# Performance work log

Measured on AMD Instinct MI355X. Metric: run time of the kernel, lower is better.

## Reference

```python
import jax, jax.numpy as jnp
import numpy as np

B, L, E, Fm, Y, K = 16, 2500, 100, 50, 8921, 10
PAD = K // 2  # floor(kernel_size/2) = 5; even kernel -> output length L+1, as in torch


def setup_inputs() -> dict:
    key = jax.random.key(0)
    ks = jax.random.split(key, 6)
    x = jax.random.normal(ks[0], (B, L, E), dtype=jnp.float32)
    target = (jax.random.uniform(ks[1], (B, Y)) < 0.01).astype(jnp.float32)
    conv_w = jax.random.normal(ks[2], (Fm, E, K), dtype=jnp.float32) * 0.05  # (out, in, k)
    conv_b = jnp.zeros((Fm,), jnp.float32)
    U_w = jax.random.normal(ks[3], (Y, Fm), dtype=jnp.float32) * 0.05
    final_w = jax.random.normal(ks[4], (Y, Fm), dtype=jnp.float32) * 0.05
    final_b = jnp.zeros((Y,), jnp.float32)
    return dict(x=x, target=target, conv_w=conv_w, conv_b=conv_b,
                U_w=U_w, final_w=final_w, final_b=final_b)


def reference(x, target, conv_w, conv_b, U_w, final_w, final_b):
    # dropout is identity in eval mode
    xc = jnp.transpose(x, (0, 2, 1))  # (B, E, L)
    h = jax.lax.conv_general_dilated(
        xc, conv_w, window_strides=(1,), padding=[(PAD, PAD)],
        dimension_numbers=('NCH', 'OIH', 'NCH'))  # (B, Fm, L+1)
    h = jnp.tanh(jnp.transpose(h + conv_b[None, :, None], (0, 2, 1)))  # (B, Lp, Fm)
    # label-wise attention: U.weight @ h^T -> (B, Y, Lp)
    scores = jnp.einsum('yf,blf->byl', U_w, h)
    alpha = jax.nn.softmax(scores, axis=2)          # (B, Y, Lp) -- dominant memory traffic
    m = jnp.einsum('byl,blf->byf', alpha, h)        # (B, Y, Fm)
    logits = jnp.sum(final_w[None, :, :] * m, axis=2) + final_b  # (B, Y)
    proba = jax.nn.log_softmax(logits, axis=1)
    # binary_cross_entropy_with_logits, mean reduction (numerically stable form)
    loss = jnp.mean(jnp.maximum(logits, 0) - logits * target
                    + jnp.log1p(jnp.exp(-jnp.abs(logits))))
    return proba, loss, alpha
```

## Files before the change

kernel.cpp:

```cpp
#include <hip/hip_runtime.h>
#include <math.h>

#define Bn 16
#define Ln 2500
#define En 100
#define FM 50
#define Yn 8921
#define KS 10
#define LP 2501
#define NT 40
#define TILE_BYTES 19456
#define TILE_SHORTS 9728
#define HT_OFF 5120
#define CH_FULL 19
#define CH_A 10
#define NW 8
#define YB 128
#define NYB 70

typedef __attribute__((ext_vector_type(8))) short short8;
typedef __attribute__((ext_vector_type(4))) float f32x4;

union S8 { short8 v; long l2[2]; short s[8]; };

__device__ __forceinline__ short f2bf(float f){
  unsigned u = __float_as_uint(f);
  unsigned r = (u + 0x7fffu + ((u >> 16) & 1u)) >> 16;
  return (short)r;
}

__device__ __forceinline__ void g2l16(const void* g, void* l){
  __builtin_amdgcn_global_load_lds(
      (const __attribute__((address_space(1))) unsigned int*)g,
      (__attribute__((address_space(3))) unsigned int*)l, 16, 0, 0);
}

__device__ __forceinline__ void stage_chunks(const char* __restrict__ gbase,
                                             char* lbase, int wave, int lane,
                                             int nch, int nw){
  for (int chunk = wave; chunk < nch; chunk += nw)
    g2l16(gbase + chunk * 1024 + lane * 16, lbase + chunk * 1024 + lane * 16);
}

__global__ void k0_wt(const float* __restrict__ cw, float* __restrict__ WT){
  int i = blockIdx.x * 256 + threadIdx.x;
  if (i < 64000){
    int f = i & 63, ek = i >> 6;
    WT[i] = (f < FM) ? cw[f * 1000 + ek] : 0.f;
  }
}

__global__ __launch_bounds__(256) void k1_conv(
    const float* __restrict__ x, const float* __restrict__ WT,
    const float* __restrict__ conv_b, short* __restrict__ Hp)
{
  int id = blockIdx.x;
  int xcd = id & 7, rr = id >> 3;
  int b   = xcd + ((rr >= NT) ? 8 : 0);
  int t   = (rr >= NT) ? rr - NT : rr;
  int tid = threadIdx.x;
  __shared__ float x_s[100 * 76];
  __shared__ short h_t[64 * 69];

  int r0 = 64 * t - 5;
  for (int d = tid; d < 7300; d += 256){
    int row = d / 100, e = d - row * 100;
    int gr = r0 + row;
    float v = (gr >= 0 && gr < Ln) ? x[((size_t)b * Ln + gr) * 100 + e] : 0.f;
    x_s[e * 76 + row] = v;
  }
  __syncthreads();

  int f = tid & 63, lsub = tid >> 6;
  float acc[16];
#pragma unroll
  for (int j = 0; j < 16; j++) acc[j] = 0.f;

  for (int e = 0; e < 100; e++){
    float xv[25];
    const float* xr = x_s + e * 76 + lsub * 16;
#pragma unroll
    for (int i = 0; i < 6; i++){
      f32x4 q = *(const f32x4*)(xr + 4 * i);
      xv[4*i+0] = q[0]; xv[4*i+1] = q[1]; xv[4*i+2] = q[2]; xv[4*i+3] = q[3];
    }
    xv[24] = xr[24];
#pragma unroll
    for (int k = 0; k < KS; k++){
      float wv = WT[(e * 10 + k) * 64 + f];
#pragma unroll
      for (int j = 0; j < 16; j++) acc[j] += wv * xv[j + k];
    }
  }

  float bias = (f < FM) ? conv_b[f] : 0.f;
  size_t tbS = (size_t)(b * NT + t) * TILE_SHORTS;
#pragma unroll
  for (int j = 0; j < 16; j++){
    int l = lsub * 16 + j;
    int lgl = 64 * t + l;
    float hv = (lgl < LP && f < FM) ? tanhf(acc[j] + bias) : 0.f;
    short hb = f2bf(hv);
    Hp[tbS + (size_t)(f >> 4) * 1280 + (size_t)l * 20 + (f & 15)] = hb;
    h_t[l * 69 + f] = hb;
  }
  __syncthreads();
  int lane = tid & 63, wave = tid >> 6;
#pragma unroll
  for (int i = 0; i < 16; i++){
    int fo = wave + 4 * i;
    Hp[tbS + HT_OFF + (size_t)fo * 72 + lane] = h_t[lane * 69 + fo];
  }
}

__device__ __forceinline__ void scores_tile(const short* __restrict__ h_s,
                                            const S8 bu[2], int c, int g, f32x4 d[4])
{
#pragma unroll
  for (int ms = 0; ms < 4; ms++){
    f32x4 acc = {0.f, 0.f, 0.f, 0.f};
#pragma unroll
    for (int kf = 0; kf < 2; kf++){
      const short* pa = h_s + (2 * kf) * 1280 + (c + 16 * ms) * 20 + 4 * g;
      S8 a;
      a.l2[0] = *(const long*)pa;
      a.l2[1] = *(const long*)(pa + 1280);
      acc = __builtin_amdgcn_mfma_f32_16x16x32_bf16(a.v, bu[kf].v, acc, 0, 0, 0);
    }
    d[ms] = acc;
  }
}

__device__ __forceinline__ void load_bu(const float* __restrict__ U_w,
                                        int ywave, int c, int g, S8 bu[2]){
  int yv = ywave + c;
#pragma unroll
  for (int kf = 0; kf < 2; kf++)
#pragma unroll
    for (int i = 0; i < 8; i++){
      int fidx = 4 * g + (i & 3) + 16 * (i >> 2) + 32 * kf;
      float v = (yv < Yn && fidx < FM) ? U_w[yv * FM + fidx] : 0.f;
      bu[kf].s[i] = f2bf(v);
    }
}

__global__ __launch_bounds__(512, 4) void k2_fused(
    const short* __restrict__ Hp,
    const float* __restrict__ U_w, const float* __restrict__ final_w,
    const float* __restrict__ final_b,
    float* __restrict__ logits, float* __restrict__ alpha_out,
    float* __restrict__ dump)
{
  int id = blockIdx.x;
  int xcd = id & 7, rr = id >> 3;
  int b   = xcd + ((rr >= NYB) ? 8 : 0);
  int y0  = ((rr >= NYB) ? rr - NYB : rr) * YB;

  int tid = threadIdx.x;
  int lane = tid & 63, wave = tid >> 6;
  int c = lane & 15, g = lane >> 4;
  int ywave = y0 + wave * 16;

  __shared__ __align__(16) short buf[2][TILE_SHORTS];
  __shared__ __align__(16) float awf[NW * 1024];

  S8 bu[2];
  load_bu(U_w, ywave, c, g, bu);

  const char* blob = (const char*)Hp + (size_t)b * NT * TILE_BYTES;

  float S = 0.f;
  {
    int cur = 0;
    stage_chunks(blob, (char*)buf[0], wave, lane, CH_A, NW);
    for (int t = 0; t < NT; t++){
      __syncthreads();
      if (t + 1 < NT)
        stage_chunks(blob + (size_t)(t + 1) * TILE_BYTES, (char*)buf[cur ^ 1], wave, lane, CH_A, NW);
      f32x4 d[4];
      scores_tile(buf[cur], bu, c, g, d);
      if (t < NT - 1){
#pragma unroll
        for (int ms = 0; ms < 4; ms++)
#pragma unroll
          for (int q = 0; q < 4; q++) S += __expf(d[ms][q]);
      } else {
#pragma unroll
        for (int ms = 0; ms < 4; ms++)
#pragma unroll
          for (int q = 0; q < 4; q++){
            int l = 64 * t + 16 * ms + 4 * g + q;
            if (l < LP) S += __expf(d[ms][q]);
          }
      }
      cur ^= 1;
    }
  }
  S += __shfl_xor(S, 16);
  S += __shfl_xor(S, 32);
  float invS = 1.f / S;
  __syncthreads();

  int Kf = (17 + 29 * b + 5 * ywave) & 31;
  int fc = (Kf + 5 * c) & 31;

  f32x4 m2[4];
#pragma unroll
  for (int fs = 0; fs < 4; fs++) m2[fs] = (f32x4){0.f, 0.f, 0.f, 0.f};

  float* aw = awf + wave * 1024;
  float* dumpf = dump + (size_t)id * 256;

  int cur = 0;
  stage_chunks(blob, (char*)buf[0], wave, lane, CH_FULL, NW);
  for (int t = 0; t < NT; t++){
    if (t == 0)      asm volatile("s_waitcnt vmcnt(0) lgkmcnt(0)" ::: "memory");
    else if (t == 1) asm volatile("s_waitcnt vmcnt(16) lgkmcnt(0)" ::: "memory");
    else             asm volatile("s_waitcnt vmcnt(4) lgkmcnt(0)" ::: "memory");
    __builtin_amdgcn_s_barrier();
    if (t + 1 < NT)
      stage_chunks(blob + (size_t)(t + 1) * TILE_BYTES, (char*)buf[cur ^ 1], wave, lane, CH_FULL, NW);
    __builtin_amdgcn_sched_barrier(0);

    const short* h_s  = buf[cur];
    const short* ht_s = buf[cur] + HT_OFF;
    f32x4 d[4];
    scores_tile(h_s, bu, c, g, d);
    float a[16];
    if (t < NT - 1){
#pragma unroll
      for (int ms = 0; ms < 4; ms++)
#pragma unroll
        for (int q = 0; q < 4; q++) a[ms * 4 + q] = __expf(d[ms][q]) * invS;
    } else {
#pragma unroll
      for (int ms = 0; ms < 4; ms++)
#pragma unroll
        for (int q = 0; q < 4; q++){
          int l = 64 * t + 16 * ms + 4 * g + q;
          a[ms * 4 + q] = (l < LP) ? __expf(d[ms][q]) * invS : 0.f;
        }
    }

#pragma unroll
    for (int kl = 0; kl < 2; kl++){
      S8 a2;
#pragma unroll
      for (int i = 0; i < 8; i++)
        a2.s[i] = f2bf(a[(2 * kl + (i >> 2)) * 4 + (i & 3)]);
#pragma unroll
      for (int fs = 0; fs < 4; fs++){
        const short* pb = ht_s + (16 * fs + c) * 72 + 4 * g + 32 * kl;
        S8 b2;
        b2.l2[0] = *(const long*)pb;
        b2.l2[1] = *(const long*)(pb + 16);
        m2[fs] = __builtin_amdgcn_mfma_f32_16x16x32_bf16(a2.v, b2.v, m2[fs], 0, 0, 0);
      }
    }

#pragma unroll
    for (int hs = 0; hs < 2; hs++){
#pragma unroll
      for (int mh = 0; mh < 2; mh++)
#pragma unroll
        for (int q = 0; q < 4; q++)
          aw[c * 64 + fc + 16 * mh + 4 * g + q] = a[(2 * hs + mh) * 4 + q];
      if (t >= 1 && t <= 38){
#pragma unroll
        for (int i = 0; i < 2; i++){
          int jj = 8 * i + (lane >> 3);
          int k4 = (lane & 7) * 4;
          int fj = (Kf + 5 * jj) & 31;
          int gcol = 64 * t + 32 * hs - fj + k4;
          f32x4 v4 = *(const f32x4*)(aw + jj * 64 + k4);
          int yj = ywave + jj;
          bool ok = (yj < Yn);
          f32x4* dst = ok ? (f32x4*)(alpha_out + (size_t)(b * Yn + yj) * LP + gcol)
                          : (f32x4*)(dumpf + 4 * lane);
          __builtin_nontemporal_store(v4, dst);
        }
      } else {
#pragma unroll
        for (int i = 0; i < 8; i++){
          int jj  = 2 * i + (lane >> 5);
          int k32 = lane & 31;
          int fj  = (Kf + 5 * jj) & 31;
          int gcol = 64 * t + 32 * hs - fj + k32;
          float v = aw[jj * 64 + k32];
          int yj = ywave + jj;
          bool ok = (gcol >= 0) & (gcol < LP) & (yj < Yn);
          float* dst = ok ? (alpha_out + (size_t)(b * Yn + yj) * LP + gcol)
                          : (dumpf + lane);
          __builtin_nontemporal_store(v, dst);
        }
      }
#pragma unroll
      for (int i = 0; i < 8; i++){
        int jj  = 2 * i + (lane >> 5);
        int k32 = lane & 31;
        int fj  = (Kf + 5 * jj) & 31;
        if (k32 < fj) aw[jj * 64 + k32] = aw[jj * 64 + 32 + k32];
      }
    }
    cur ^= 1;
  }

  float part[4];
#pragma unroll
  for (int q = 0; q < 4; q++){
    int yy = ywave + 4 * g + q;
    float p = 0.f;
    if (yy < Yn){
#pragma unroll
      for (int fs = 0; fs < 4; fs++){
        int fcol = fs * 16 + c;
        if (fcol < FM) p += m2[fs][q] * final_w[yy * FM + fcol];
      }
    }
#pragma unroll
    for (int off = 1; off <= 8; off <<= 1) p += __shfl_xor(p, off);
    part[q] = p;
  }
  if (c == 0){
#pragma unroll
    for (int q = 0; q < 4; q++){
      int yy = ywave + 4 * g + q;
      if (yy < Yn) logits[(size_t)b * Yn + yy] = part[q] + final_b[yy];
    }
  }
}

__global__ __launch_bounds__(256) void k3_lsm(
    const float* __restrict__ logits, const float* __restrict__ target,
    float* __restrict__ proba, float* __restrict__ lossp)
{
  int b = blockIdx.x, tid = threadIdx.x;
  int lane = tid & 63, wave = tid >> 6;
  __shared__ float red[4];
  const float* lg = logits + (size_t)b * Yn;
  const float* tg = target + (size_t)b * Yn;

  float m = -INFINITY;
  for (int y = tid; y < Yn; y += 256) m = fmaxf(m, lg[y]);
#pragma unroll
  for (int off = 1; off <= 32; off <<= 1) m = fmaxf(m, __shfl_xor(m, off));
  if (lane == 0) red[wave] = m;
  __syncthreads();
  m = fmaxf(fmaxf(red[0], red[1]), fmaxf(red[2], red[3]));
  __syncthreads();

  float s = 0.f;
  for (int y = tid; y < Yn; y += 256) s += __expf(lg[y] - m);
#pragma unroll
  for (int off = 1; off <= 32; off <<= 1) s += __shfl_xor(s, off);
  if (lane == 0) red[wave] = s;
  __syncthreads();
  s = red[0] + red[1] + red[2] + red[3];
  __syncthreads();
  float lse = m + logf(s);

  float ls = 0.f;
  for (int y = tid; y < Yn; y += 256){
    float xx = lg[y];
    proba[(size_t)b * Yn + y] = xx - lse;
    ls += fmaxf(xx, 0.f) - xx * tg[y] + log1pf(__expf(-fabsf(xx)));
  }
#pragma unroll
  for (int off = 1; off <= 32; off <<= 1) ls += __shfl_xor(ls, off);
  if (lane == 0) red[wave] = ls;
  __syncthreads();
  if (tid == 0) lossp[b] = red[0] + red[1] + red[2] + red[3];
}

__global__ void k4_loss(const float* __restrict__ lossp, float* __restrict__ out){
  if (threadIdx.x == 0){
    float s = 0.f;
    for (int i = 0; i < Bn; i++) s += lossp[i];
    out[142736] = s / 142736.f;
  }
}

extern "C" void kernel_launch(void* const* d_in, const int* in_sizes, int n_in,
                              void* d_out, int out_size, void* d_ws, size_t ws_size,
                              hipStream_t stream)
{
  const float* x       = (const float*)d_in[0];
  const float* target  = (const float*)d_in[1];
  const float* conv_w  = (const float*)d_in[2];
  const float* conv_b  = (const float*)d_in[3];
  const float* U_w     = (const float*)d_in[4];
  const float* final_w = (const float*)d_in[5];
  const float* final_b = (const float*)d_in[6];
  float* out = (float*)d_out;

  char* ws = (char*)d_ws;
  short* Hp     = (short*)(ws);
  float* WT     = (float*)(ws + 12451840);
  float* logits = (float*)(ws + 12707840);
  float* lossp  = (float*)(ws + 13278784);
  float* dump   = (float*)(ws + 13278848);

  float* proba     = out;
  float* alpha_out = out + 142737;

  k0_wt<<<dim3(250), dim3(256), 0, stream>>>(conv_w, WT);
  k1_conv<<<dim3(8 * 2 * NT), dim3(256), 0, stream>>>(x, WT, conv_b, Hp);
  k2_fused<<<dim3(8 * 2 * NYB), dim3(512), 0, stream>>>(Hp, U_w, final_w, final_b,
                                                        logits, alpha_out, dump);
  k3_lsm<<<dim3(Bn), dim3(256), 0, stream>>>(logits, target, proba, lossp);
  k4_loss<<<dim3(1), dim3(64), 0, stream>>>(lossp, out);
}
```

Baseline: 596.2 us.

## Drop transposed H copy; swap MFMA operands to reuse single H layout

The conv kernel no longer writes a second transposed copy of the bf16 hidden tile, which halves the per-tile blob size and the global-to-LDS staging traffic in the attention kernel. The alpha·H product now swaps MFMA operands (H as A, alpha as B), gathering H from the original layout with eight scalar LDS reads per fragment instead of two 64-bit reads. The logits epilogue is rewritten to match the transposed accumulator layout. This trades less memory traffic and LDS footprint for more LDS read instructions and possible bank conflicts in the inner loop.

```diff
diff --git a/kernel.cpp b/kernel.cpp
--- a/kernel.cpp
+++ b/kernel.cpp
@@ -9,11 +9,9 @@
 #define KS 10
 #define LP 2501
 #define NT 40
-#define TILE_BYTES 19456
-#define TILE_SHORTS 9728
-#define HT_OFF 5120
-#define CH_FULL 19
-#define CH_A 10
+#define TILE_SHORTS 5120
+#define TILE_BYTES 10240
+#define CH 10
 #define NW 8
 #define YB 128
 #define NYB 70
@@ -36,9 +34,8 @@
 }
 
 __device__ __forceinline__ void stage_chunks(const char* __restrict__ gbase,
-                                             char* lbase, int wave, int lane,
-                                             int nch, int nw){
-  for (int chunk = wave; chunk < nch; chunk += nw)
+                                             char* lbase, int wave, int lane){
+  for (int chunk = wave; chunk < CH; chunk += NW)
     g2l16(gbase + chunk * 1024 + lane * 16, lbase + chunk * 1024 + lane * 16);
 }
 
@@ -60,7 +57,6 @@
   int t   = (rr >= NT) ? rr - NT : rr;
   int tid = threadIdx.x;
   __shared__ float x_s[100 * 76];
-  __shared__ short h_t[64 * 69];
 
   int r0 = 64 * t - 5;
   for (int d = tid; d < 7300; d += 256){
@@ -100,16 +96,7 @@
     int l = lsub * 16 + j;
     int lgl = 64 * t + l;
     float hv = (lgl < LP && f < FM) ? tanhf(acc[j] + bias) : 0.f;
-    short hb = f2bf(hv);
-    Hp[tbS + (size_t)(f >> 4) * 1280 + (size_t)l * 20 + (f & 15)] = hb;
-    h_t[l * 69 + f] = hb;
-  }
-  __syncthreads();
-  int lane = tid & 63, wave = tid >> 6;
-#pragma unroll
-  for (int i = 0; i < 16; i++){
-    int fo = wave + 4 * i;
-    Hp[tbS + HT_OFF + (size_t)fo * 72 + lane] = h_t[lane * 69 + fo];
+    Hp[tbS + (size_t)(f >> 4) * 1280 + (size_t)l * 20 + (f & 15)] = f2bf(hv);
   }
 }
 
@@ -172,11 +159,11 @@
   float S = 0.f;
   {
     int cur = 0;
-    stage_chunks(blob, (char*)buf[0], wave, lane, CH_A, NW);
+    stage_chunks(blob, (char*)buf[0], wave, lane);
     for (int t = 0; t < NT; t++){
       __syncthreads();
       if (t + 1 < NT)
-        stage_chunks(blob + (size_t)(t + 1) * TILE_BYTES, (char*)buf[cur ^ 1], wave, lane, CH_A, NW);
+        stage_chunks(blob + (size_t)(t + 1) * TILE_BYTES, (char*)buf[cur ^ 1], wave, lane);
       f32x4 d[4];
       scores_tile(buf[cur], bu, c, g, d);
       if (t < NT - 1){
@@ -212,18 +199,17 @@
   float* dumpf = dump + (size_t)id * 256;
 
   int cur = 0;
-  stage_chunks(blob, (char*)buf[0], wave, lane, CH_FULL, NW);
+  stage_chunks(blob, (char*)buf[0], wave, lane);
   for (int t = 0; t < NT; t++){
     if (t == 0)      asm volatile("s_waitcnt vmcnt(0) lgkmcnt(0)" ::: "memory");
     else if (t == 1) asm volatile("s_waitcnt vmcnt(16) lgkmcnt(0)" ::: "memory");
     else             asm volatile("s_waitcnt vmcnt(4) lgkmcnt(0)" ::: "memory");
     __builtin_amdgcn_s_barrier();
     if (t + 1 < NT)
-      stage_chunks(blob + (size_t)(t + 1) * TILE_BYTES, (char*)buf[cur ^ 1], wave, lane, CH_FULL, NW);
+      stage_chunks(blob + (size_t)(t + 1) * TILE_BYTES, (char*)buf[cur ^ 1], wave, lane);
     __builtin_amdgcn_sched_barrier(0);
 
-    const short* h_s  = buf[cur];
-    const short* ht_s = buf[cur] + HT_OFF;
+    const short* h_s = buf[cur];
     f32x4 d[4];
     scores_tile(h_s, bu, c, g, d);
     float a[16];
@@ -250,11 +236,12 @@
         a2.s[i] = f2bf(a[(2 * kl + (i >> 2)) * 4 + (i & 3)]);
 #pragma unroll
       for (int fs = 0; fs < 4; fs++){
-        const short* pb = ht_s + (16 * fs + c) * 72 + 4 * g + 32 * kl;
-        S8 b2;
-        b2.l2[0] = *(const long*)pb;
-        b2.l2[1] = *(const long*)(pb + 16);
-        m2[fs] = __builtin_amdgcn_mfma_f32_16x16x32_bf16(a2.v, b2.v, m2[fs], 0, 0, 0);
+        const short* pa2 = h_s + fs * 1280 + (4 * g + 32 * kl) * 20 + c;
+        S8 av;
+#pragma unroll
+        for (int i = 0; i < 8; i++)
+          av.s[i] = pa2[(i & 3) * 20 + (i >> 2) * 320];
+        m2[fs] = __builtin_amdgcn_mfma_f32_16x16x32_bf16(av.v, a2.v, m2[fs], 0, 0, 0);
       }
     }
 
@@ -305,29 +292,21 @@
     cur ^= 1;
   }
 
-  float part[4];
-#pragma unroll
-  for (int q = 0; q < 4; q++){
-    int yy = ywave + 4 * g + q;
-    float p = 0.f;
-    if (yy < Yn){
-#pragma unroll
-      for (int fs = 0; fs < 4; fs++){
-        int fcol = fs * 16 + c;
-        if (fcol < FM) p += m2[fs][q] * final_w[yy * FM + fcol];
-      }
-    }
-#pragma unroll
-    for (int off = 1; off <= 8; off <<= 1) p += __shfl_xor(p, off);
-    part[q] = p;
-  }
-  if (c == 0){
-#pragma unroll
-    for (int q = 0; q < 4; q++){
-      int yy = ywave + 4 * g + q;
-      if (yy < Yn) logits[(size_t)b * Yn + yy] = part[q] + final_b[yy];
-    }
-  }
+  float p = 0.f;
+  int yv = ywave + c;
+  if (yv < Yn){
+#pragma unroll
+    for (int fs = 0; fs < 4; fs++)
+#pragma unroll
+      for (int q = 0; q < 4; q++){
+        int fcol = 16 * fs + 4 * g + q;
+        if (fcol < FM) p += m2[fs][q] * final_w[yv * FM + fcol];
+      }
+  }
+  p += __shfl_xor(p, 16);
+  p += __shfl_xor(p, 32);
+  if (g == 0 && yv < Yn)
+    logits[(size_t)b * Yn + yv] = p + final_b[yv];
 }
 
 __global__ __launch_bounds__(256) void k3_lsm(
@@ -395,10 +374,10 @@
 
   char* ws = (char*)d_ws;
   short* Hp     = (short*)(ws);
-  float* WT     = (float*)(ws + 12451840);
-  float* logits = (float*)(ws + 12707840);
-  float* lossp  = (float*)(ws + 13278784);
-  float* dump   = (float*)(ws + 13278848);
+  float* WT     = (float*)(ws + 6553600);
+  float* logits = (float*)(ws + 6809600);
+  float* lossp  = (float*)(ws + 7380544);
+  float* dump   = (float*)(ws + 7380608);
 
   float* proba     = out;
   float* alpha_out = out + 142737;
```

After: 585.1 us, median of 2. About the same (-1.9%).
